# Kernel tuning notes

Hardware: AMD Instinct MI355X
Metric: run time of the kernel (lower is better)

The kernel has to match this reference:

```python
import jax, jax.numpy as jnp
import numpy as np

N, E, G = 100000, 1600000, 128
IN, HID, HEADS, EDIM, OUT = 16, 32, 4, 8, 4
HC = HEADS * HID


def _p(k, shape):
    return jax.random.normal(k, shape, jnp.float32) * 0.1


def setup_inputs():
    key = jax.random.key(0)
    ks = list(jax.random.split(key, 24))
    nxt = iter(ks)
    d = dict(
        x=jax.random.normal(next(nxt), (N, IN), jnp.float32),
        edge_index=jax.random.randint(next(nxt), (2, E), 0, N),
        edge_attr=jax.random.normal(next(nxt), (E, EDIM), jnp.float32),
        batch=jnp.sort(jax.random.randint(next(nxt), (N,), 0, G)),
    )
    # conv1: in=IN -> heads*hid
    d['wl1'] = _p(next(nxt), (IN, HC));  d['bl1'] = jnp.zeros((HC,), jnp.float32)
    d['wr1'] = _p(next(nxt), (IN, HC));  d['br1'] = jnp.zeros((HC,), jnp.float32)
    d['we1'] = _p(next(nxt), (EDIM, HC)); d['att1'] = _p(next(nxt), (HEADS, HID)); d['bc1'] = jnp.zeros((HC,), jnp.float32)
    # conv2: in=HC -> heads*hid
    d['wl2'] = _p(next(nxt), (HC, HC));  d['bl2'] = jnp.zeros((HC,), jnp.float32)
    d['wr2'] = _p(next(nxt), (HC, HC));  d['br2'] = jnp.zeros((HC,), jnp.float32)
    d['we2'] = _p(next(nxt), (EDIM, HC)); d['att2'] = _p(next(nxt), (HEADS, HID)); d['bc2'] = jnp.zeros((HC,), jnp.float32)
    # conv3: in=HC -> 1*hid (heads=1)
    d['wl3'] = _p(next(nxt), (HC, HID)); d['bl3'] = jnp.zeros((HID,), jnp.float32)
    d['wr3'] = _p(next(nxt), (HC, HID)); d['br3'] = jnp.zeros((HID,), jnp.float32)
    d['we3'] = _p(next(nxt), (EDIM, HID)); d['att3'] = _p(next(nxt), (1, HID)); d['bc3'] = jnp.zeros((HID,), jnp.float32)
    d['w_fc1'] = _p(next(nxt), (HID, 2 * HID)); d['b_fc1'] = jnp.zeros((2 * HID,), jnp.float32)
    d['w_fc2'] = _p(next(nxt), (2 * HID, OUT)); d['b_fc2'] = jnp.zeros((OUT,), jnp.float32)
    return d


def _gatv2(x, src, dst, eattr, wl, bl, wr, br, we, att, bias, n):
    # PyG GATv2Conv: e_ij = a^T . leaky_relu(Wl x_j + Wr x_i + We e_ij)
    H, C = att.shape
    xl = (x @ wl + bl).reshape(-1, H, C)  # source transform [N,H,C]
    xr = (x @ wr + br).reshape(-1, H, C)  # target transform [N,H,C]
    ea = (eattr @ we).reshape(-1, H, C)   # edge transform   [E,H,C]
    e = jax.nn.leaky_relu(xl[src] + xr[dst] + ea, 0.2)  # [E,H,C]
    logit = jnp.einsum('ehc,hc->eh', e, att)            # [E,H]
    m = jax.ops.segment_max(logit, dst, num_segments=n)
    p = jnp.exp(logit - m[dst])
    s = jax.ops.segment_sum(p, dst, num_segments=n)
    alpha = p / (s[dst] + 1e-16)                        # segment softmax per dst
    out = jax.ops.segment_sum(xl[src] * alpha[:, :, None], dst, num_segments=n)
    return out.reshape(n, H * C) + bias


def reference(x, edge_index, edge_attr, batch,
              wl1, bl1, wr1, br1, we1, att1, bc1,
              wl2, bl2, wr2, br2, we2, att2, bc2,
              wl3, bl3, wr3, br3, we3, att3, bc3,
              w_fc1, b_fc1, w_fc2, b_fc2):
    n = x.shape[0]
    src, dst = edge_index[0], edge_index[1]
    # add_self_loops=True with fill_value='mean' (mean of incoming edge_attr per node)
    ones_e = jnp.ones((src.shape[0],), x.dtype)
    cnt = jax.ops.segment_sum(ones_e, dst, num_segments=n)
    loop_attr = jax.ops.segment_sum(edge_attr, dst, num_segments=n) / jnp.maximum(cnt, 1.0)[:, None]
    ar = jnp.arange(n)
    src_a = jnp.concatenate([src, ar])
    dst_a = jnp.concatenate([dst, ar])
    ea = jnp.concatenate([edge_attr, loop_attr], axis=0)

    h = jax.nn.elu(_gatv2(x, src_a, dst_a, ea, wl1, bl1, wr1, br1, we1, att1, bc1, n))
    h = jax.nn.elu(_gatv2(h, src_a, dst_a, ea, wl2, bl2, wr2, br2, we2, att2, bc2, n))
    h = jax.nn.elu(_gatv2(h, src_a, dst_a, ea, wl3, bl3, wr3, br3, we3, att3, bc3, n))

    # global mean pool over graphs
    gs = jax.ops.segment_sum(h, batch, num_segments=G)
    gc = jax.ops.segment_sum(jnp.ones((n,), h.dtype), batch, num_segments=G)
    g = gs / jnp.maximum(gc, 1.0)[:, None]

    g = jax.nn.elu(g @ w_fc1 + b_fc1)
    return g @ w_fc2 + b_fc2
```

## Files before the change

### kernel.cpp

```cpp
#include <hip/hip_runtime.h>
#include <cstdint>
#include <type_traits>

constexpr int GNUM = 128;

typedef _Float16 h2 __attribute__((ext_vector_type(2)));
typedef _Float16 h4 __attribute__((ext_vector_type(4)));
typedef _Float16 h8 __attribute__((ext_vector_type(8)));
typedef float f4 __attribute__((ext_vector_type(4)));

template <int CTRL>
__device__ __forceinline__ float dppadd(float v) {
  union U { float f; int i; };
  U u, r;
  u.f = v;
  r.i = __builtin_amdgcn_update_dpp(0, u.i, CTRL, 0xF, 0xF, true);
  return v + r.f;
}

__device__ __forceinline__ float hdot2(h2 a, h2 b, float c) {
#if __has_builtin(__builtin_amdgcn_fdot2)
  return __builtin_amdgcn_fdot2(a, b, c, false);
#else
  return c + (float)a[0] * (float)b[0] + (float)a[1] * (float)b[1];
#endif
}


__global__ __launch_bounds__(256) void rank_hist_kernel(const int* __restrict__ dst,
                                                        int* __restrict__ cnt,
                                                        int* __restrict__ rank, int E) {
  int i = blockIdx.x * 256 + threadIdx.x;
  if (i >= E) return;
  rank[i] = atomicAdd(&cnt[dst[i]], 1);
}

__global__ __launch_bounds__(256) void scan_part_kernel(const int* __restrict__ cnt,
                                                        int* __restrict__ bpart, int n) {
  __shared__ int red[256];
  int base = blockIdx.x * 512;
  int t = threadIdx.x;
  int s = 0;
  int i0 = base + t, i1 = base + 256 + t;
  if (i0 < n) s += cnt[i0] + 1;
  if (i1 < n) s += cnt[i1] + 1;
  red[t] = s;
  __syncthreads();
  for (int off = 128; off > 0; off >>= 1) {
    if (t < off) red[t] += red[t + off];
    __syncthreads();
  }
  if (t == 0) bpart[blockIdx.x] = red[0];
}

__global__ __launch_bounds__(1024) void scan_top_kernel(const int* __restrict__ bpart,
                                                        int* __restrict__ boff,
                                                        int* __restrict__ row_ptr,
                                                        const int* __restrict__ batch,
                                                        int* __restrict__ gstart,
                                                        int B, int n) {
  __shared__ int buf[1024];
  int t = threadIdx.x;
  buf[t] = (t < B) ? bpart[t] : 0;
  __syncthreads();
  for (int off = 1; off < 1024; off <<= 1) {
    int v = (t >= off) ? buf[t - off] : 0;
    __syncthreads();
    buf[t] += v;
    __syncthreads();
  }
  if (t < B) boff[t] = (t == 0) ? 0 : buf[t - 1];
  if (t == 0) row_ptr[n] = buf[1023];
  if (t <= GNUM) {
    int lo = 0, hi = n;
    while (lo < hi) {
      int mid = (lo + hi) >> 1;
      if (batch[mid] < t) lo = mid + 1; else hi = mid;
    }
    gstart[t] = lo;
  }
}

__global__ __launch_bounds__(256) void scan_write_kernel(const int* __restrict__ cnt,
                                                         const int* __restrict__ boff,
                                                         int* __restrict__ row_ptr, int n) {
  __shared__ int red[256];
  int base = blockIdx.x * 512;
  int t = threadIdx.x;
  int i0 = base + 2 * t, i1 = base + 2 * t + 1;
  int v0 = (i0 < n) ? cnt[i0] + 1 : 0;
  int v1 = (i1 < n) ? cnt[i1] + 1 : 0;
  int val = v0 + v1;
  red[t] = val;
  __syncthreads();
  for (int off = 1; off < 256; off <<= 1) {
    int u = (t >= off) ? red[t - off] : 0;
    __syncthreads();
    red[t] += u;
    __syncthreads();
  }
  int o = boff[blockIdx.x] + red[t] - val;
  if (i0 < n) row_ptr[i0] = o;
  if (i1 < n) row_ptr[i1] = o + v0;
}

__global__ __launch_bounds__(256) void place_kernel(const int* __restrict__ src,
                                                    const int* __restrict__ dst,
                                                    const int* __restrict__ rank,
                                                    const int* __restrict__ row_ptr,
                                                    const float* __restrict__ ea,
                                                    int* __restrict__ csr_src,
                                                    _Float16* __restrict__ ea_csr, int E) {
  int i = blockIdx.x * 256 + threadIdx.x;
  if (i >= E) return;
  int d = dst[i];
  int p = row_ptr[d] + rank[i];
  csr_src[p] = src[i];
  float4 e0 = *(const float4*)&ea[(size_t)i * 8];
  float4 e1 = *(const float4*)&ea[(size_t)i * 8 + 4];
  h8 v;
  v[0] = (_Float16)e0.x; v[1] = (_Float16)e0.y; v[2] = (_Float16)e0.z; v[3] = (_Float16)e0.w;
  v[4] = (_Float16)e1.x; v[5] = (_Float16)e1.y; v[6] = (_Float16)e1.z; v[7] = (_Float16)e1.w;
  *(h8*)&ea_csr[(size_t)p * 8] = v;
}

__global__ __launch_bounds__(256) void selfloop_kernel(const int* __restrict__ row_ptr,
                                                       int* __restrict__ csr_src,
                                                       _Float16* __restrict__ ea_csr, int n) {
  int idx = blockIdx.x * 256 + threadIdx.x;
  int i = idx >> 3, c = idx & 7;
  if (i >= n) return;
  int s = row_ptr[i], e = row_ptr[i + 1] - 1;
  float a = 0.f;
  for (int j = s; j < e; j++) a += (float)ea_csr[(size_t)j * 8 + c];
  float inv = 1.f / fmaxf((float)(e - s), 1.f);
  ea_csr[(size_t)e * 8 + c] = (_Float16)(a * inv);
  if (c == 0) csr_src[e] = i;
}

__global__ __launch_bounds__(256) void pack_all_kernel(
    const float* __restrict__ wl1, _Float16* __restrict__ p1l,
    const float* __restrict__ wr1, _Float16* __restrict__ p1r,
    const float* __restrict__ wl2, _Float16* __restrict__ p2l,
    const float* __restrict__ wr2, _Float16* __restrict__ p2r,
    const float* __restrict__ wl3, _Float16* __restrict__ p3l,
    const float* __restrict__ wr3, _Float16* __restrict__ p3r) {
  int y = blockIdx.y;
  const float* w; _Float16* wp; int Kreal, Kpad, NC;
  switch (y) {
    case 0: w = wl1; wp = p1l; Kreal = 16;  Kpad = 32;  NC = 128; break;
    case 1: w = wr1; wp = p1r; Kreal = 16;  Kpad = 32;  NC = 128; break;
    case 2: w = wl2; wp = p2l; Kreal = 128; Kpad = 128; NC = 128; break;
    case 3: w = wr2; wp = p2r; Kreal = 128; Kpad = 128; NC = 128; break;
    case 4: w = wl3; wp = p3l; Kreal = 128; Kpad = 128; NC = 32;  break;
    default: w = wr3; wp = p3r; Kreal = 128; Kpad = 128; NC = 32; break;
  }
  int KB = Kpad / 32;
  int total = (NC / 16) * KB * 64;
  int idx = blockIdx.x * 256 + threadIdx.x;
  if (idx >= total) return;
  int lane = idx & 63;
  int blk = idx >> 6;
  int nt = blk / KB, kb = blk % KB;
  int col = nt * 16 + (lane & 15);
  int krow = kb * 32 + (lane >> 4) * 8;
  h8 v;
#pragma unroll
  for (int j = 0; j < 8; j++)
    v[j] = (krow + j < Kreal) ? (_Float16)w[(size_t)(krow + j) * NC + col] : (_Float16)0.f;
  *(h8*)&wp[(size_t)idx * 8] = v;
}


template <int K, int NCOLS>
__global__ __launch_bounds__(256) void k1m_kernel(const _Float16* __restrict__ x,
                                                  const _Float16* __restrict__ wp0,
                                                  const float* __restrict__ b0,
                                                  _Float16* __restrict__ out0,
                                                  const _Float16* __restrict__ wp1,
                                                  const float* __restrict__ b1,
                                                  _Float16* __restrict__ out1, int n) {
  constexpr int NT = NCOLS / 16, KB = K / 32;
  const _Float16* wp = blockIdx.y ? wp1 : wp0;
  const float* b = blockIdx.y ? b1 : b0;
  _Float16* out = blockIdx.y ? out1 : out0;

  int tid = threadIdx.x;
  int wave = tid >> 6, lane = tid & 63;
  int m = lane & 15, quad = lane >> 4;
  int node0 = blockIdx.x * 64 + wave * 16;

  h8 afrag[KB];
  int anode = node0 + m;
  if (anode < n) {
#pragma unroll
    for (int kb = 0; kb < KB; kb++)
      afrag[kb] = *(const h8*)&x[(size_t)anode * K + kb * 32 + quad * 8];
  } else {
#pragma unroll
    for (int kb = 0; kb < KB; kb++) afrag[kb] = (h8)(_Float16)0.f;
  }

  f4 acc[NT] = {};
#pragma unroll
  for (int nt = 0; nt < NT; nt++) {
#pragma unroll
    for (int kb = 0; kb < KB; kb++) {
      h8 bfrag = *(const h8*)&wp[((size_t)(nt * KB + kb) * 64 + lane) * 8];
      acc[nt] = __builtin_amdgcn_mfma_f32_16x16x32_f16(afrag[kb], bfrag, acc[nt], 0, 0, 0);
    }
  }

#pragma unroll
  for (int nt = 0; nt < NT; nt++) {
#pragma unroll
    for (int r = 0; r < 4; r++) {
      int row = node0 + quad * 4 + r;
      if (row < n) {
        int col = nt * 16 + m;
        out[(size_t)row * NCOLS + col] = (_Float16)(acc[nt][r] + b[col]);
      }
    }
  }
}

template <int NCOLS>
__global__ __launch_bounds__(256) void k1m16_kernel(const float* __restrict__ x,
                                                    const _Float16* __restrict__ wp0,
                                                    const float* __restrict__ b0,
                                                    _Float16* __restrict__ out0,
                                                    const _Float16* __restrict__ wp1,
                                                    const float* __restrict__ b1,
                                                    _Float16* __restrict__ out1, int n) {
  constexpr int NT = NCOLS / 16;
  const _Float16* wp = blockIdx.y ? wp1 : wp0;
  const float* b = blockIdx.y ? b1 : b0;
  _Float16* out = blockIdx.y ? out1 : out0;

  int tid = threadIdx.x;
  int wave = tid >> 6, lane = tid & 63;
  int m = lane & 15, quad = lane >> 4;
  int node0 = blockIdx.x * 64 + wave * 16;

  int anode = node0 + m;
  h8 afrag = (h8)(_Float16)0.f;
  if (anode < n && quad < 2) {
    float4 v0 = *(const float4*)&x[(size_t)anode * 16 + quad * 8];
    float4 v1 = *(const float4*)&x[(size_t)anode * 16 + quad * 8 + 4];
    afrag[0] = (_Float16)v0.x; afrag[1] = (_Float16)v0.y;
    afrag[2] = (_Float16)v0.z; afrag[3] = (_Float16)v0.w;
    afrag[4] = (_Float16)v1.x; afrag[5] = (_Float16)v1.y;
    afrag[6] = (_Float16)v1.z; afrag[7] = (_Float16)v1.w;
  }

  f4 acc[NT] = {};
#pragma unroll
  for (int nt = 0; nt < NT; nt++) {
    h8 bfrag = *(const h8*)&wp[((size_t)nt * 64 + lane) * 8];
    acc[nt] = __builtin_amdgcn_mfma_f32_16x16x32_f16(afrag, bfrag, acc[nt], 0, 0, 0);
  }

#pragma unroll
  for (int nt = 0; nt < NT; nt++) {
#pragma unroll
    for (int r = 0; r < 4; r++) {
      int row = node0 + quad * 4 + r;
      if (row < n) {
        int col = nt * 16 + m;
        out[(size_t)row * NCOLS + col] = (_Float16)(acc[nt][r] + b[col]);
      }
    }
  }
}

__global__ __launch_bounds__(256) void k2w_kernel(
    const _Float16* __restrict__ xl, const _Float16* __restrict__ xr,
    const int* __restrict__ row_ptr, const int* __restrict__ csr_src,
    const _Float16* __restrict__ ea_csr, const float* __restrict__ we,
    const float* __restrict__ att, const float* __restrict__ bc,
    _Float16* __restrict__ out, int n) {
  int tid = threadIdx.x;
  int lane = tid & 63;
  int node = blockIdx.x * 4 + (tid >> 6);
  if (node >= n) return;
  int c0 = lane << 1;

  int start = __builtin_amdgcn_readfirstlane(row_ptr[node]);
  int end   = __builtin_amdgcn_readfirstlane(row_ptr[node + 1]);
  int len = end - start;
  int pairs = (len + 1) >> 1;

  int j1 = (start + 1 < end) ? start + 1 : start;
  float m1 = (start + 1 < end) ? 1.f : 0.f;
  int s0 = __builtin_amdgcn_readfirstlane(csr_src[start]);
  int s1 = __builtin_amdgcn_readfirstlane(csr_src[j1]);
  h8 e0 = *(const h8*)&ea_csr[(size_t)start * 8];
  h8 e1 = *(const h8*)&ea_csr[(size_t)j1 * 8];

  h2 w2[8];
#pragma unroll
  for (int k = 0; k < 8; k++) {
    float2 v = *(const float2*)&we[k * 128 + c0];
    w2[k] = h2{(_Float16)v.x, (_Float16)v.y};
  }
  const float LOG2E = 1.44269504088896f;
  float2 av = *(const float2*)&att[c0];
  h2 a2 = h2{(_Float16)(av.x * LOG2E), (_Float16)(av.y * LOG2E)};
  h2 xr2 = *(const h2*)&xr[(size_t)node * 128 + c0];
  const h2 p2 = h2{(_Float16)0.2f, (_Float16)0.2f};

  h2 x0 = *(const h2*)&xl[(uint32_t)s0 * 128u + (uint32_t)c0];
  h2 x1 = *(const h2*)&xl[(uint32_t)s1 * 128u + (uint32_t)c0];

  int jn = start + 2;
  int k0 = (jn < end) ? jn : start;
  int k1 = (jn + 1 < end) ? jn + 1 : k0;
  float m1n = (jn + 1 < end) ? 1.f : 0.f;
  int s0n = __builtin_amdgcn_readfirstlane(csr_src[k0]);
  int s1n = __builtin_amdgcn_readfirstlane(csr_src[k1]);
  h8 e0n = *(const h8*)&ea_csr[(size_t)k0 * 8];
  h8 e1n = *(const h8*)&ea_csr[(size_t)k1 * 8];

  float s = 0.f, acc0 = 0.f, acc1 = 0.f;

#pragma unroll 2
  for (int p = 0; p < pairs; p++) {
    int ja = start + 2 * (p + 2);
    int ka0 = (ja < end) ? ja : start;
    int ka1 = (ja + 1 < end) ? ja + 1 : ka0;
    float m1a = (ja + 1 < end) ? 1.f : 0.f;
    int s0a = __builtin_amdgcn_readfirstlane(csr_src[ka0]);
    int s1a = __builtin_amdgcn_readfirstlane(csr_src[ka1]);
    h8 e0a = *(const h8*)&ea_csr[(size_t)ka0 * 8];
    h8 e1a = *(const h8*)&ea_csr[(size_t)ka1 * 8];

    h2 x0n = *(const h2*)&xl[(uint32_t)s0n * 128u + (uint32_t)c0];
    h2 x1n = *(const h2*)&xl[(uint32_t)s1n * 128u + (uint32_t)c0];

    h2 t0 = x0 + xr2;
    h2 t1 = x1 + xr2;
#pragma unroll
    for (int k = 0; k < 8; k++) {
      t0 += h2{e0[k], e0[k]} * w2[k];
      t1 += h2{e1[k], e1[k]} * w2[k];
    }
    t0 = __builtin_elementwise_max(t0, t0 * p2);
    t1 = __builtin_elementwise_max(t1, t1 * p2);
    float part0 = hdot2(t0, a2, 0.f);
    float part1 = hdot2(t1, a2, 0.f);
    part0 = dppadd<0xB1>(part0);   part1 = dppadd<0xB1>(part1);
    part0 = dppadd<0x4E>(part0);   part1 = dppadd<0x4E>(part1);
    part0 = dppadd<0x141>(part0);  part1 = dppadd<0x141>(part1);
    part0 = dppadd<0x140>(part0);  part1 = dppadd<0x140>(part1);
    float pe0 = __builtin_amdgcn_exp2f(part0);
    float pe1 = __builtin_amdgcn_exp2f(part1) * m1;
    s += pe0 + pe1;
    acc0 += pe0 * (float)x0[0] + pe1 * (float)x1[0];
    acc1 += pe0 * (float)x0[1] + pe1 * (float)x1[1];

    x0 = x0n; x1 = x1n; e0 = e0n; e1 = e1n; m1 = m1n;
    s0n = s0a; s1n = s1a; e0n = e0a; e1n = e1a; m1n = m1a;
  }

  float inv = 1.f / (s + 1e-16f);
  float2 bv = *(const float2*)&bc[c0];
  float v0 = acc0 * inv + bv.x;
  float v1 = acc1 * inv + bv.y;
  v0 = v0 > 0.f ? v0 : (__expf(v0) - 1.f);
  v1 = v1 > 0.f ? v1 : (__expf(v1) - 1.f);
  *(h2*)&out[(size_t)node * 128 + c0] = h2{(_Float16)v0, (_Float16)v1};
}

template <int H>
__global__ __launch_bounds__(128) void k2_kernel(
    const _Float16* __restrict__ xl, const _Float16* __restrict__ xr,
    const int* __restrict__ row_ptr, const int* __restrict__ csr_src,
    const _Float16* __restrict__ ea_csr, const float* __restrict__ we,
    const float* __restrict__ att, const float* __restrict__ bc,
    _Float16* __restrict__ out, int n) {
  constexpr int HC = H * 32;
  constexpr int NL = HC / 4;
  constexpr int NPB = 128 / NL;

  int tid = threadIdx.x;
  int ln = tid / NL, q = tid % NL;
  int c0 = 4 * q;
  int node = blockIdx.x * NPB + ln;
  if (node >= n) return;

  h2 w2[8][2];
#pragma unroll
  for (int k = 0; k < 8; k++) {
    float4 v = *(const float4*)&we[k * HC + c0];
    w2[k][0] = h2{(_Float16)v.x, (_Float16)v.y};
    w2[k][1] = h2{(_Float16)v.z, (_Float16)v.w};
  }
  const float LOG2E = 1.44269504088896f;
  float4 av = *(const float4*)&att[c0];
  h2 a0 = h2{(_Float16)(av.x * LOG2E), (_Float16)(av.y * LOG2E)};
  h2 a1 = h2{(_Float16)(av.z * LOG2E), (_Float16)(av.w * LOG2E)};
  h4 xrh = *(const h4*)&xr[(size_t)node * HC + c0];
  h2 xr0 = h2{xrh[0], xrh[1]}, xr1 = h2{xrh[2], xrh[3]};
  const h2 p2 = h2{(_Float16)0.2f, (_Float16)0.2f};

  float acc[4] = {0.f, 0.f, 0.f, 0.f};
  float s = 0.f;

  int start = row_ptr[node], end = row_ptr[node + 1];
  int len = end - start;
  int pairs = (len + 1) >> 1;

  int j1 = (start + 1 < end) ? start + 1 : start;
  float m1 = (start + 1 < end) ? 1.f : 0.f;
  int s0 = csr_src[start], s1 = csr_src[j1];
  h8 e0 = *(const h8*)&ea_csr[(size_t)start * 8];
  h8 e1 = *(const h8*)&ea_csr[(size_t)j1 * 8];
  h4 x0 = *(const h4*)&xl[(size_t)s0 * HC + c0];
  h4 x1 = *(const h4*)&xl[(size_t)s1 * HC + c0];

#pragma unroll 2
  for (int p = 0; p < pairs; p++) {
    int jn = start + 2 * (p + 1);
    int k0 = (jn < end) ? jn : start;
    int k1 = (jn + 1 < end) ? jn + 1 : k0;
    float nm1 = (jn + 1 < end) ? 1.f : 0.f;
    int ns0 = csr_src[k0], ns1 = csr_src[k1];
    h8 ne0 = *(const h8*)&ea_csr[(size_t)k0 * 8];
    h8 ne1 = *(const h8*)&ea_csr[(size_t)k1 * 8];

    h2 t00 = h2{x0[0], x0[1]} + xr0;
    h2 t01 = h2{x0[2], x0[3]} + xr1;
    h2 t10 = h2{x1[0], x1[1]} + xr0;
    h2 t11 = h2{x1[2], x1[3]} + xr1;
#pragma unroll
    for (int k = 0; k < 8; k++) {
      h2 ev0 = h2{e0[k], e0[k]};
      h2 ev1 = h2{e1[k], e1[k]};
      t00 += ev0 * w2[k][0];
      t01 += ev0 * w2[k][1];
      t10 += ev1 * w2[k][0];
      t11 += ev1 * w2[k][1];
    }
    t00 = __builtin_elementwise_max(t00, t00 * p2);
    t01 = __builtin_elementwise_max(t01, t01 * p2);
    t10 = __builtin_elementwise_max(t10, t10 * p2);
    t11 = __builtin_elementwise_max(t11, t11 * p2);
    float part0 = hdot2(t00, a0, hdot2(t01, a1, 0.f));
    float part1 = hdot2(t10, a0, hdot2(t11, a1, 0.f));

    h4 nx0 = *(const h4*)&xl[(size_t)ns0 * HC + c0];
    h4 nx1 = *(const h4*)&xl[(size_t)ns1 * HC + c0];

    part0 = dppadd<0xB1>(part0);   part1 = dppadd<0xB1>(part1);
    part0 = dppadd<0x4E>(part0);   part1 = dppadd<0x4E>(part1);
    part0 = dppadd<0x141>(part0);  part1 = dppadd<0x141>(part1);
    float pe0 = __builtin_amdgcn_exp2f(part0);
    float pe1 = __builtin_amdgcn_exp2f(part1) * m1;
    s += pe0 + pe1;
#pragma unroll
    for (int i = 0; i < 4; i++)
      acc[i] += pe0 * (float)x0[i] + pe1 * (float)x1[i];

    s0 = ns0; s1 = ns1; e0 = ne0; e1 = ne1; x0 = nx0; x1 = nx1; m1 = nm1;
  }

  float inv = 1.f / (s + 1e-16f);
  h4 o;
#pragma unroll
  for (int i = 0; i < 4; i++) {
    float v = acc[i] * inv + bc[c0 + i];
    o[i] = (_Float16)(v > 0.f ? v : (__expf(v) - 1.f));
  }
  *(h4*)&out[(size_t)node * HC + c0] = o;
}

__global__ __launch_bounds__(256) void poolfc_kernel(const _Float16* __restrict__ h,
                                                     const int* __restrict__ gstart,
                                                     const float* __restrict__ w1,
                                                     const float* __restrict__ b1,
                                                     const float* __restrict__ w2,
                                                     const float* __restrict__ b2,
                                                     float* __restrict__ out) {
  __shared__ float redx[256];
  __shared__ float redy[256];
  __shared__ float g[32];
  __shared__ float a1[64];
  int gi = blockIdx.x;
  int t = threadIdx.x;
  int s = gstart[gi], e = gstart[gi + 1];
  int cp = t & 15, rg = t >> 4;
  float ax = 0.f, ay = 0.f;
  for (int i = s + rg; i < e; i += 16) {
    h2 v = *(const h2*)&h[(size_t)i * 32 + cp * 2];
    ax += (float)v[0]; ay += (float)v[1];
  }
  redx[t] = ax; redy[t] = ay;
  __syncthreads();
  if (t < 128) { redx[t] += redx[t + 128]; redy[t] += redy[t + 128]; }
  __syncthreads();
  if (t < 64) { redx[t] += redx[t + 64]; redy[t] += redy[t + 64]; }
  __syncthreads();
  if (t < 32) { redx[t] += redx[t + 32]; redy[t] += redy[t + 32]; }
  __syncthreads();
  if (t < 16) {
    float inv = 1.f / fmaxf((float)(e - s), 1.f);
    g[2 * t]     = (redx[t] + redx[t + 16]) * inv;
    g[2 * t + 1] = (redy[t] + redy[t + 16]) * inv;
  }
  __syncthreads();
  if (t < 64) {
    float v = b1[t];
    for (int k = 0; k < 32; k++) v += g[k] * w1[k * 64 + t];
    a1[t] = v > 0.f ? v : (__expf(v) - 1.f);
  }
  __syncthreads();
  if (t < 4) {
    float o = b2[t];
    for (int k = 0; k < 64; k++) o += a1[k] * w2[k * 4 + t];
    out[gi * 4 + t] = o;
  }
}


extern "C" void kernel_launch(void* const* d_in, const int* in_sizes, int n_in,
                              void* d_out, int out_size, void* d_ws, size_t ws_size,
                              hipStream_t stream) {
  const float* x     = (const float*)d_in[0];
  const int*   ei    = (const int*)d_in[1];
  const float* eattr = (const float*)d_in[2];
  const int*   batch = (const int*)d_in[3];
  const float *wl1 = (const float*)d_in[4],  *bl1 = (const float*)d_in[5];
  const float *wr1 = (const float*)d_in[6],  *br1 = (const float*)d_in[7];
  const float *we1 = (const float*)d_in[8],  *at1 = (const float*)d_in[9];
  const float *bc1 = (const float*)d_in[10];
  const float *wl2 = (const float*)d_in[11], *bl2 = (const float*)d_in[12];
  const float *wr2 = (const float*)d_in[13], *br2 = (const float*)d_in[14];
  const float *we2 = (const float*)d_in[15], *at2 = (const float*)d_in[16];
  const float *bc2 = (const float*)d_in[17];
  const float *wl3 = (const float*)d_in[18], *bl3 = (const float*)d_in[19];
  const float *wr3 = (const float*)d_in[20], *br3 = (const float*)d_in[21];
  const float *we3 = (const float*)d_in[22], *at3 = (const float*)d_in[23];
  const float *bc3 = (const float*)d_in[24];
  const float *wf1 = (const float*)d_in[25], *bf1 = (const float*)d_in[26];
  const float *wf2 = (const float*)d_in[27], *bf2 = (const float*)d_in[28];

  int N = in_sizes[0] / 16;
  int E = in_sizes[1] / 2;
  const int* srcp = ei;
  const int* dstp = ei + E;
  int EA = E + N;
  int NB = (N + 511) / 512;

  char* wsb = (char*)d_ws;
  size_t off = 0;
  auto alloc = [&](size_t bytes) -> char* {
    char* p = wsb + off;
    off += (bytes + 255) & ~(size_t)255;
    return p;
  };
  int*       cnt     = (int*)alloc((size_t)N * 4);
  int*       row_ptr = (int*)alloc((size_t)(N + 1) * 4);
  int*       rank    = (int*)alloc((size_t)E * 4);
  int*       bpart   = (int*)alloc((size_t)1024 * 4);
  int*       boff    = (int*)alloc((size_t)1024 * 4);
  int*       csr_src = (int*)alloc((size_t)EA * 4);
  _Float16*  ea_csr  = (_Float16*)alloc((size_t)EA * 8 * 2);
  _Float16*  xl      = (_Float16*)alloc((size_t)N * 128 * 2);
  _Float16*  xr      = (_Float16*)alloc((size_t)N * 128 * 2);
  _Float16*  h16     = (_Float16*)alloc((size_t)N * 128 * 2);
  _Float16*  h3      = (_Float16*)alloc((size_t)N * 32 * 2);
  int*       gstart  = (int*)alloc((size_t)(GNUM + 1) * 4);
  _Float16*  wp1l    = (_Float16*)alloc((size_t)32 * 128 * 2);
  _Float16*  wp1r    = (_Float16*)alloc((size_t)32 * 128 * 2);
  _Float16*  wp2l    = (_Float16*)alloc((size_t)128 * 128 * 2);
  _Float16*  wp2r    = (_Float16*)alloc((size_t)128 * 128 * 2);
  _Float16*  wp3l    = (_Float16*)alloc((size_t)128 * 32 * 2);
  _Float16*  wp3r    = (_Float16*)alloc((size_t)128 * 32 * 2);

  hipMemsetAsync(cnt, 0, (size_t)N * 4, stream);

  rank_hist_kernel<<<(E + 255) / 256, 256, 0, stream>>>(dstp, cnt, rank, E);
  scan_part_kernel<<<NB, 256, 0, stream>>>(cnt, bpart, N);
  scan_top_kernel<<<1, 1024, 0, stream>>>(bpart, boff, row_ptr, batch, gstart, NB, N);
  scan_write_kernel<<<NB, 256, 0, stream>>>(cnt, boff, row_ptr, N);
  place_kernel<<<(E + 255) / 256, 256, 0, stream>>>(srcp, dstp, rank, row_ptr, eattr,
                                                    csr_src, ea_csr, E);
  selfloop_kernel<<<(N * 8 + 255) / 256, 256, 0, stream>>>(row_ptr, csr_src, ea_csr, N);
  pack_all_kernel<<<dim3(8, 6), 256, 0, stream>>>(wl1, wp1l, wr1, wp1r,
                                                  wl2, wp2l, wr2, wp2r,
                                                  wl3, wp3l, wr3, wp3r);

  k1m16_kernel<128><<<dim3((N + 63) / 64, 2), 256, 0, stream>>>(
      x, wp1l, bl1, xl, wp1r, br1, xr, N);
  k2w_kernel<<<(N + 3) / 4, 256, 0, stream>>>(xl, xr, row_ptr, csr_src, ea_csr,
                                              we1, at1, bc1, h16, N);
  k1m_kernel<128, 128><<<dim3((N + 63) / 64, 2), 256, 0, stream>>>(
      h16, wp2l, bl2, xl, wp2r, br2, xr, N);
  k2w_kernel<<<(N + 3) / 4, 256, 0, stream>>>(xl, xr, row_ptr, csr_src, ea_csr,
                                              we2, at2, bc2, h16, N);
  k1m_kernel<128, 32><<<dim3((N + 63) / 64, 2), 256, 0, stream>>>(
      h16, wp3l, bl3, xl, wp3r, br3, xr, N);
  k2_kernel<1><<<(N + 15) / 16, 128, 0, stream>>>(xl, xr, row_ptr, csr_src, ea_csr,
                                                  we3, at3, bc3, h3, N);

  poolfc_kernel<<<GNUM, 256, 0, stream>>>(h3, gstart, wf1, bf1, wf2, bf2, (float*)d_out);
}
```

Measured before the change: 666.1 us.

## Fuse left/right projection GEMMs per block and repartition layer-3 aggregation across waves

The node projection kernels now compute both the source and target transforms in one block, reusing the loaded A fragments instead of launching a second grid dimension that reloads the input rows. The single-head layer-3 aggregation is rewritten so each wavefront handles one node, with four lane groups of 16 processing different edges in parallel and a cross-group shuffle reduction at the end. This is meant to cut redundant input loads and raise memory-level parallelism on the gather-bound last layer. In exchange it doubles accumulator registers per thread and halves the projection grid, which may lower occupancy.

```diff
diff --git a/kernel.cpp b/kernel.cpp
--- a/kernel.cpp
+++ b/kernel.cpp
@@ -173,17 +173,14 @@
 
 
 template <int K, int NCOLS>
-__global__ __launch_bounds__(256) void k1m_kernel(const _Float16* __restrict__ x,
-                                                  const _Float16* __restrict__ wp0,
-                                                  const float* __restrict__ b0,
-                                                  _Float16* __restrict__ out0,
-                                                  const _Float16* __restrict__ wp1,
-                                                  const float* __restrict__ b1,
-                                                  _Float16* __restrict__ out1, int n) {
+__global__ __launch_bounds__(256) void k1mf_kernel(const _Float16* __restrict__ x,
+                                                   const _Float16* __restrict__ wpL,
+                                                   const float* __restrict__ bL,
+                                                   _Float16* __restrict__ outL,
+                                                   const _Float16* __restrict__ wpR,
+                                                   const float* __restrict__ bR,
+                                                   _Float16* __restrict__ outR, int n) {
   constexpr int NT = NCOLS / 16, KB = K / 32;
-  const _Float16* wp = blockIdx.y ? wp1 : wp0;
-  const float* b = blockIdx.y ? b1 : b0;
-  _Float16* out = blockIdx.y ? out1 : out0;
 
   int tid = threadIdx.x;
   int wave = tid >> 6, lane = tid & 63;
@@ -201,13 +198,15 @@
     for (int kb = 0; kb < KB; kb++) afrag[kb] = (h8)(_Float16)0.f;
   }
 
-  f4 acc[NT] = {};
+  f4 accL[NT] = {}, accR[NT] = {};
 #pragma unroll
   for (int nt = 0; nt < NT; nt++) {
 #pragma unroll
     for (int kb = 0; kb < KB; kb++) {
-      h8 bfrag = *(const h8*)&wp[((size_t)(nt * KB + kb) * 64 + lane) * 8];
-      acc[nt] = __builtin_amdgcn_mfma_f32_16x16x32_f16(afrag[kb], bfrag, acc[nt], 0, 0, 0);
+      h8 bfL = *(const h8*)&wpL[((size_t)(nt * KB + kb) * 64 + lane) * 8];
+      accL[nt] = __builtin_amdgcn_mfma_f32_16x16x32_f16(afrag[kb], bfL, accL[nt], 0, 0, 0);
+      h8 bfR = *(const h8*)&wpR[((size_t)(nt * KB + kb) * 64 + lane) * 8];
+      accR[nt] = __builtin_amdgcn_mfma_f32_16x16x32_f16(afrag[kb], bfR, accR[nt], 0, 0, 0);
     }
   }
 
@@ -218,24 +217,22 @@
       int row = node0 + quad * 4 + r;
       if (row < n) {
         int col = nt * 16 + m;
-        out[(size_t)row * NCOLS + col] = (_Float16)(acc[nt][r] + b[col]);
+        outL[(size_t)row * NCOLS + col] = (_Float16)(accL[nt][r] + bL[col]);
+        outR[(size_t)row * NCOLS + col] = (_Float16)(accR[nt][r] + bR[col]);
       }
     }
   }
 }
 
 template <int NCOLS>
-__global__ __launch_bounds__(256) void k1m16_kernel(const float* __restrict__ x,
-                                                    const _Float16* __restrict__ wp0,
-                                                    const float* __restrict__ b0,
-                                                    _Float16* __restrict__ out0,
-                                                    const _Float16* __restrict__ wp1,
-                                                    const float* __restrict__ b1,
-                                                    _Float16* __restrict__ out1, int n) {
+__global__ __launch_bounds__(256) void k1m16f_kernel(const float* __restrict__ x,
+                                                     const _Float16* __restrict__ wpL,
+                                                     const float* __restrict__ bL,
+                                                     _Float16* __restrict__ outL,
+                                                     const _Float16* __restrict__ wpR,
+                                                     const float* __restrict__ bR,
+                                                     _Float16* __restrict__ outR, int n) {
   constexpr int NT = NCOLS / 16;
-  const _Float16* wp = blockIdx.y ? wp1 : wp0;
-  const float* b = blockIdx.y ? b1 : b0;
-  _Float16* out = blockIdx.y ? out1 : out0;
 
   int tid = threadIdx.x;
   int wave = tid >> 6, lane = tid & 63;
@@ -253,11 +250,13 @@
     afrag[6] = (_Float16)v1.z; afrag[7] = (_Float16)v1.w;
   }
 
-  f4 acc[NT] = {};
+  f4 accL[NT] = {}, accR[NT] = {};
 #pragma unroll
   for (int nt = 0; nt < NT; nt++) {
-    h8 bfrag = *(const h8*)&wp[((size_t)nt * 64 + lane) * 8];
-    acc[nt] = __builtin_amdgcn_mfma_f32_16x16x32_f16(afrag, bfrag, acc[nt], 0, 0, 0);
+    h8 bfL = *(const h8*)&wpL[((size_t)nt * 64 + lane) * 8];
+    accL[nt] = __builtin_amdgcn_mfma_f32_16x16x32_f16(afrag, bfL, accL[nt], 0, 0, 0);
+    h8 bfR = *(const h8*)&wpR[((size_t)nt * 64 + lane) * 8];
+    accR[nt] = __builtin_amdgcn_mfma_f32_16x16x32_f16(afrag, bfR, accR[nt], 0, 0, 0);
   }
 
 #pragma unroll
@@ -267,7 +266,8 @@
       int row = node0 + quad * 4 + r;
       if (row < n) {
         int col = nt * 16 + m;
-        out[(size_t)row * NCOLS + col] = (_Float16)(acc[nt][r] + b[col]);
+        outL[(size_t)row * NCOLS + col] = (_Float16)(accL[nt][r] + bL[col]);
+        outR[(size_t)row * NCOLS + col] = (_Float16)(accR[nt][r] + bR[col]);
       }
     }
   }
@@ -371,107 +371,87 @@
   *(h2*)&out[(size_t)node * 128 + c0] = h2{(_Float16)v0, (_Float16)v1};
 }
 
-template <int H>
-__global__ __launch_bounds__(128) void k2_kernel(
+__global__ __launch_bounds__(256) void k2w1_kernel(
     const _Float16* __restrict__ xl, const _Float16* __restrict__ xr,
     const int* __restrict__ row_ptr, const int* __restrict__ csr_src,
     const _Float16* __restrict__ ea_csr, const float* __restrict__ we,
     const float* __restrict__ att, const float* __restrict__ bc,
     _Float16* __restrict__ out, int n) {
-  constexpr int HC = H * 32;
-  constexpr int NL = HC / 4;
-  constexpr int NPB = 128 / NL;
-
   int tid = threadIdx.x;
-  int ln = tid / NL, q = tid % NL;
-  int c0 = 4 * q;
-  int node = blockIdx.x * NPB + ln;
+  int lane = tid & 63;
+  int node = blockIdx.x * 4 + (tid >> 6);
   if (node >= n) return;
-
-  h2 w2[8][2];
+  int g = lane >> 4;
+  int c0 = (lane & 15) << 1;
+
+  int start = __builtin_amdgcn_readfirstlane(row_ptr[node]);
+  int end   = __builtin_amdgcn_readfirstlane(row_ptr[node + 1]);
+  int last = end - 1;
+  int iters = (end - start + 3) >> 2;
+
+  int j0 = start + g;
+  int ks = (j0 < end) ? j0 : last;
+  float m = (j0 < end) ? 1.f : 0.f;
+  int sp = csr_src[ks];
+  h8 e = *(const h8*)&ea_csr[(size_t)ks * 8];
+
+  h2 w2[8];
 #pragma unroll
   for (int k = 0; k < 8; k++) {
-    float4 v = *(const float4*)&we[k * HC + c0];
-    w2[k][0] = h2{(_Float16)v.x, (_Float16)v.y};
-    w2[k][1] = h2{(_Float16)v.z, (_Float16)v.w};
+    float2 v = *(const float2*)&we[k * 32 + c0];
+    w2[k] = h2{(_Float16)v.x, (_Float16)v.y};
   }
   const float LOG2E = 1.44269504088896f;
-  float4 av = *(const float4*)&att[c0];
-  h2 a0 = h2{(_Float16)(av.x * LOG2E), (_Float16)(av.y * LOG2E)};
-  h2 a1 = h2{(_Float16)(av.z * LOG2E), (_Float16)(av.w * LOG2E)};
-  h4 xrh = *(const h4*)&xr[(size_t)node * HC + c0];
-  h2 xr0 = h2{xrh[0], xrh[1]}, xr1 = h2{xrh[2], xrh[3]};
+  float2 av = *(const float2*)&att[c0];
+  h2 a2 = h2{(_Float16)(av.x * LOG2E), (_Float16)(av.y * LOG2E)};
+  h2 xr2 = *(const h2*)&xr[(size_t)node * 32 + c0];
   const h2 p2 = h2{(_Float16)0.2f, (_Float16)0.2f};
 
-  float acc[4] = {0.f, 0.f, 0.f, 0.f};
-  float s = 0.f;
-
-  int start = row_ptr[node], end = row_ptr[node + 1];
-  int len = end - start;
-  int pairs = (len + 1) >> 1;
-
-  int j1 = (start + 1 < end) ? start + 1 : start;
-  float m1 = (start + 1 < end) ? 1.f : 0.f;
-  int s0 = csr_src[start], s1 = csr_src[j1];
-  h8 e0 = *(const h8*)&ea_csr[(size_t)start * 8];
-  h8 e1 = *(const h8*)&ea_csr[(size_t)j1 * 8];
-  h4 x0 = *(const h4*)&xl[(size_t)s0 * HC + c0];
-  h4 x1 = *(const h4*)&xl[(size_t)s1 * HC + c0];
+  h2 xv = *(const h2*)&xl[(uint32_t)sp * 32u + (uint32_t)c0];
+
+  float s = 0.f, acc0 = 0.f, acc1 = 0.f;
 
 #pragma unroll 2
-  for (int p = 0; p < pairs; p++) {
-    int jn = start + 2 * (p + 1);
-    int k0 = (jn < end) ? jn : start;
-    int k1 = (jn + 1 < end) ? jn + 1 : k0;
-    float nm1 = (jn + 1 < end) ? 1.f : 0.f;
-    int ns0 = csr_src[k0], ns1 = csr_src[k1];
-    h8 ne0 = *(const h8*)&ea_csr[(size_t)k0 * 8];
-    h8 ne1 = *(const h8*)&ea_csr[(size_t)k1 * 8];
-
-    h2 t00 = h2{x0[0], x0[1]} + xr0;
-    h2 t01 = h2{x0[2], x0[3]} + xr1;
-    h2 t10 = h2{x1[0], x1[1]} + xr0;
-    h2 t11 = h2{x1[2], x1[3]} + xr1;
-#pragma unroll
-    for (int k = 0; k < 8; k++) {
-      h2 ev0 = h2{e0[k], e0[k]};
-      h2 ev1 = h2{e1[k], e1[k]};
-      t00 += ev0 * w2[k][0];
-      t01 += ev0 * w2[k][1];
-      t10 += ev1 * w2[k][0];
-      t11 += ev1 * w2[k][1];
-    }
-    t00 = __builtin_elementwise_max(t00, t00 * p2);
-    t01 = __builtin_elementwise_max(t01, t01 * p2);
-    t10 = __builtin_elementwise_max(t10, t10 * p2);
-    t11 = __builtin_elementwise_max(t11, t11 * p2);
-    float part0 = hdot2(t00, a0, hdot2(t01, a1, 0.f));
-    float part1 = hdot2(t10, a0, hdot2(t11, a1, 0.f));
-
-    h4 nx0 = *(const h4*)&xl[(size_t)ns0 * HC + c0];
-    h4 nx1 = *(const h4*)&xl[(size_t)ns1 * HC + c0];
-
-    part0 = dppadd<0xB1>(part0);   part1 = dppadd<0xB1>(part1);
-    part0 = dppadd<0x4E>(part0);   part1 = dppadd<0x4E>(part1);
-    part0 = dppadd<0x141>(part0);  part1 = dppadd<0x141>(part1);
-    float pe0 = __builtin_amdgcn_exp2f(part0);
-    float pe1 = __builtin_amdgcn_exp2f(part1) * m1;
-    s += pe0 + pe1;
-#pragma unroll
-    for (int i = 0; i < 4; i++)
-      acc[i] += pe0 * (float)x0[i] + pe1 * (float)x1[i];
-
-    s0 = ns0; s1 = ns1; e0 = ne0; e1 = ne1; x0 = nx0; x1 = nx1; m1 = nm1;
-  }
-
-  float inv = 1.f / (s + 1e-16f);
-  h4 o;
-#pragma unroll
-  for (int i = 0; i < 4; i++) {
-    float v = acc[i] * inv + bc[c0 + i];
-    o[i] = (_Float16)(v > 0.f ? v : (__expf(v) - 1.f));
-  }
-  *(h4*)&out[(size_t)node * HC + c0] = o;
+  for (int p = 0; p < iters; p++) {
+    int jn = start + 4 * (p + 1) + g;
+    int kn = (jn < end) ? jn : last;
+    float mn = (jn < end) ? 1.f : 0.f;
+    int spn = csr_src[kn];
+    h8 en = *(const h8*)&ea_csr[(size_t)kn * 8];
+
+    h2 t = xv + xr2;
+#pragma unroll
+    for (int k = 0; k < 8; k++) t += h2{e[k], e[k]} * w2[k];
+    t = __builtin_elementwise_max(t, t * p2);
+    float part = hdot2(t, a2, 0.f);
+
+    h2 xvn = *(const h2*)&xl[(uint32_t)spn * 32u + (uint32_t)c0];
+
+    part = dppadd<0xB1>(part);
+    part = dppadd<0x4E>(part);
+    part = dppadd<0x141>(part);
+    part = dppadd<0x140>(part);
+    float pe = __builtin_amdgcn_exp2f(part) * m;
+    s += pe;
+    acc0 += pe * (float)xv[0];
+    acc1 += pe * (float)xv[1];
+
+    xv = xvn; e = en; m = mn;
+  }
+
+  s    += __shfl_xor(s, 16, 64);    s    += __shfl_xor(s, 32, 64);
+  acc0 += __shfl_xor(acc0, 16, 64); acc0 += __shfl_xor(acc0, 32, 64);
+  acc1 += __shfl_xor(acc1, 16, 64); acc1 += __shfl_xor(acc1, 32, 64);
+
+  if (g == 0) {
+    float inv = 1.f / (s + 1e-16f);
+    float2 bv = *(const float2*)&bc[c0];
+    float v0 = acc0 * inv + bv.x;
+    float v1 = acc1 * inv + bv.y;
+    v0 = v0 > 0.f ? v0 : (__expf(v0) - 1.f);
+    v1 = v1 > 0.f ? v1 : (__expf(v1) - 1.f);
+    *(h2*)&out[(size_t)node * 32 + c0] = h2{(_Float16)v0, (_Float16)v1};
+  }
 }
 
 __global__ __launch_bounds__(256) void poolfc_kernel(const _Float16* __restrict__ h,
@@ -590,18 +570,18 @@
                                                   wl2, wp2l, wr2, wp2r,
                                                   wl3, wp3l, wr3, wp3r);
 
-  k1m16_kernel<128><<<dim3((N + 63) / 64, 2), 256, 0, stream>>>(
+  k1m16f_kernel<128><<<(N + 63) / 64, 256, 0, stream>>>(
       x, wp1l, bl1, xl, wp1r, br1, xr, N);
   k2w_kernel<<<(N + 3) / 4, 256, 0, stream>>>(xl, xr, row_ptr, csr_src, ea_csr,
                                               we1, at1, bc1, h16, N);
-  k1m_kernel<128, 128><<<dim3((N + 63) / 64, 2), 256, 0, stream>>>(
+  k1mf_kernel<128, 128><<<(N + 63) / 64, 256, 0, stream>>>(
       h16, wp2l, bl2, xl, wp2r, br2, xr, N);
   k2w_kernel<<<(N + 3) / 4, 256, 0, stream>>>(xl, xr, row_ptr, csr_src, ea_csr,
                                               we2, at2, bc2, h16, N);
-  k1m_kernel<128, 32><<<dim3((N + 63) / 64, 2), 256, 0, stream>>>(
+  k1mf_kernel<128, 32><<<(N + 63) / 64, 256, 0, stream>>>(
       h16, wp3l, bl3, xl, wp3r, br3, xr, N);
-  k2_kernel<1><<<(N + 15) / 16, 128, 0, stream>>>(xl, xr, row_ptr, csr_src, ea_csr,
-                                                  we3, at3, bc3, h3, N);
+  k2w1_kernel<<<(N + 3) / 4, 256, 0, stream>>>(xl, xr, row_ptr, csr_src, ea_csr,
+                                               we3, at3, bc3, h3, N);
 
   poolfc_kernel<<<GNUM, 256, 0, stream>>>(h3, gstart, wf1, bf1, wf2, bf2, (float*)d_out);
 }
```

Result: slower. 703.1 us (+5.6%).
